# Optimization experiments

Hardware: AMD Instinct MI355X
Metric: run time of the kernel (lower is better)

## Reference

```python
import jax, jax.numpy as jnp
import numpy as np

K_NN = 3  # pointnet2 relation default k=3


def setup_inputs() -> dict:
    key = jax.random.key(0)
    k1, k2, k3 = jax.random.split(key, 3)
    B, N, S, C = 4, 16384, 4096, 256
    q = jax.random.normal(k1, (B, N, 3), dtype=jnp.float32)
    k = jax.random.normal(k2, (B, S, 3), dtype=jnp.float32)
    v = jax.random.normal(k3, (B, S, C), dtype=jnp.float32)
    return {"q": q, "k": k, "v": v}


def reference(q, k, v):
    # squared pairwise distance: ||q||^2 - 2 q.k + ||k||^2  -> [B, N, S]
    d = (
        jnp.sum(q * q, axis=-1, keepdims=True)
        - 2.0 * jnp.einsum("bnd,bsd->bns", q, k)
        + jnp.sum(k * k, axis=-1)[:, None, :]
    )
    # 3 nearest neighbors (smallest distances)
    neg_d, idx = jax.lax.top_k(-d, K_NN)          # [B, N, 3]
    dists = -neg_d
    recip = 1.0 / (dists + 1e-8)
    weight = recip / jnp.sum(recip, axis=-1, keepdims=True)  # [B, N, 3]
    # score is zero except at idx; scatter+dense matmul == gather-weighted sum
    B = q.shape[0]
    vg = v[jnp.arange(B)[:, None, None], idx]     # [B, N, 3, C]
    extract = jnp.einsum("bnk,bnkc->bnc", weight, vg)  # [B, N, C]
    return jnp.transpose(extract, (0, 2, 1))      # [B, C, N] (embed is identity)
```

## Files before the change

### kernel.cpp

```cpp
#include <hip/hip_runtime.h>

#define BB 4
#define NN 16384
#define SS 4096
#define CC 256
#define TLD 132

typedef float f32x4 __attribute__((ext_vector_type(4)));

__device__ __forceinline__ bool lexlt(float da, int ia, float db, int ib) {
  return (da < db) || ((da == db) && (ia < ib));
}

__global__ __launch_bounds__(256, 4) void scan_kernel(
    const float* __restrict__ qg, const float* __restrict__ kg,
    float4* __restrict__ dpart, int4* __restrict__ ipart) {
#pragma clang fp contract(off)
  __shared__ __align__(16) float4 kpts[1024];

  const int tid = threadIdx.x;
  const int blk = blockIdx.x;
  const int b = blk >> 8;
  const int seg = (blk >> 6) & 3;
  const int n0 = (blk & 63) << 8;
  const int wv = tid >> 6;
  const int lane = tid & 63;
  const int q = n0 + wv * 64 + lane;

  {
    const float* kb = kg + ((long)b * SS + (long)seg * 1024) * 3;
    const float4* src = (const float4*)kb + tid * 3;
    float4 f0 = src[0], f1 = src[1], f2 = src[2];
    float px[4] = {f0.x, f0.w, f1.z, f2.y};
    float py[4] = {f0.y, f1.x, f1.w, f2.z};
    float pz[4] = {f0.z, f1.y, f2.x, f2.w};
#pragma unroll
    for (int m = 0; m < 4; ++m) {
      float kk = (px[m] * px[m] + py[m] * py[m]) + pz[m] * pz[m];
      kpts[tid * 4 + m] = make_float4(px[m], py[m], pz[m], kk);
    }
  }

  const float* qp = qg + ((long)b * NN + q) * 3;
  float qx = qp[0], qy = qp[1], qz = qp[2];
  float qq = (qx * qx + qy * qy) + qz * qz;
  float d0 = 3.4e38f, d1 = 3.4e38f, d2 = 3.4e38f;
  int i0 = 0, i1 = 0, i2 = 0;
  __syncthreads();

  const int sb = seg * 1024;

#pragma unroll 4
  for (int i = 0; i < 256; ++i) {
    float4 kp = kpts[i];
    float dot = (qx * kp.x + qy * kp.y) + qz * kp.z;
    float d = __builtin_fmaf(dot, -2.0f, qq) + kp.w;
    const int s = sb + i;
    bool k2 = d < d2;
    bool k1 = d < d1;
    bool k0 = d < d0;
    float nd2 = __builtin_amdgcn_fmed3f(d, d1, d2);
    float nd1 = __builtin_amdgcn_fmed3f(d, d0, d1);
    float nd0 = fminf(d, d0);
    i2 = k1 ? i1 : (k2 ? s : i2);
    i1 = k0 ? i0 : (k1 ? s : i1);
    i0 = k0 ? s : i0;
    d2 = nd2; d1 = nd1; d0 = nd0;
  }

  for (int c = 1; c < 4; ++c) {
    const float tau = d2;
    const int base = c * 256;
#pragma unroll 4
    for (int i = 0; i < 256; ++i) {
      float4 kp = kpts[base + i];
      float dot = (qx * kp.x + qy * kp.y) + qz * kp.z;
      float d = __builtin_fmaf(dot, -2.0f, qq) + kp.w;
      if (__builtin_expect(__any(d < tau), 0)) {
        const int s = sb + base + i;
        bool k2 = d < d2;
        bool k1 = d < d1;
        bool k0 = d < d0;
        float nd2 = __builtin_amdgcn_fmed3f(d, d1, d2);
        float nd1 = __builtin_amdgcn_fmed3f(d, d0, d1);
        float nd0 = fminf(d, d0);
        i2 = k1 ? i1 : (k2 ? s : i2);
        i1 = k0 ? i0 : (k1 ? s : i1);
        i0 = k0 ? s : i0;
        d2 = nd2; d1 = nd1; d0 = nd0;
      }
    }
  }

  long gid = (long)b * NN + q;
  dpart[gid * 4 + seg] = make_float4(d0, d1, d2, 0.0f);
  ipart[gid * 4 + seg] = make_int4(i0, i1, i2, 0);
}

__global__ __launch_bounds__(256, 4) void gather_kernel(
    const float* __restrict__ vg, const float4* __restrict__ dpart,
    const int4* __restrict__ ipart, float* __restrict__ outg) {
#pragma clang fp contract(off)
  __shared__ __align__(16) float tile[64 * TLD];
  __shared__ float sw[64][3];
  __shared__ int si[64][3];

  const int tid = threadIdx.x;
  const int bid = blockIdx.x;
  const int xcd = bid & 7;
  const int b = xcd >> 1;
  const int chunk = xcd & 1;
  const int nblk = bid >> 3;
  const int n0 = nblk << 6;

  if (tid < 64) {
    long gid = (long)b * NN + n0 + tid;
    float D0 = 3.4e38f, D1 = 3.4e38f, D2 = 3.4e38f;
    int I0 = -1, I1 = -1, I2 = -1;
#pragma unroll
    for (int seg = 0; seg < 4; ++seg) {
      float4 dv = dpart[gid * 4 + seg];
      int4 iv = ipart[gid * 4 + seg];
      float ds_[3] = {dv.x, dv.y, dv.z};
      int is_[3] = {iv.x, iv.y, iv.z};
      for (int r = 0; r < 3; ++r) {
        float d = ds_[r];
        int s = is_[r];
        if (lexlt(d, s, D2, I2)) {
          if (lexlt(d, s, D1, I1)) {
            D2 = D1; I2 = I1;
            if (lexlt(d, s, D0, I0)) { D1 = D0; I1 = I0; D0 = d; I0 = s; }
            else { D1 = d; I1 = s; }
          } else { D2 = d; I2 = s; }
        }
      }
    }
    float r0 = 1.0f / (D0 + 1e-8f);
    float r1 = 1.0f / (D1 + 1e-8f);
    float r2 = 1.0f / (D2 + 1e-8f);
    float rs = (r0 + r1) + r2;
    sw[tid][0] = r0 / rs; sw[tid][1] = r1 / rs; sw[tid][2] = r2 / rs;
    si[tid][0] = I0; si[tid][1] = I1; si[tid][2] = I2;
  }
  __syncthreads();

  const int wv = tid >> 6;
  const int lane = tid & 63;
  const int qh = lane >> 5;
  const int slot = lane & 31;
  const float* vb = vg + (long)b * SS * CC + chunk * 128;

#pragma unroll 4
  for (int it = 0; it < 8; ++it) {
    int qs = wv * 16 + it * 2 + qh;
    float w0 = sw[qs][0], w1 = sw[qs][1], w2 = sw[qs][2];
    const float4* r0p = (const float4*)(vb + (long)si[qs][0] * CC);
    const float4* r1p = (const float4*)(vb + (long)si[qs][1] * CC);
    const float4* r2p = (const float4*)(vb + (long)si[qs][2] * CC);
    float4 a0 = r0p[slot], a1 = r1p[slot], a2 = r2p[slot];
    float4 acc;
    acc.x = (w0 * a0.x + w1 * a1.x) + w2 * a2.x;
    acc.y = (w0 * a0.y + w1 * a1.y) + w2 * a2.y;
    acc.z = (w0 * a0.z + w1 * a1.z) + w2 * a2.z;
    acc.w = (w0 * a0.w + w1 * a1.w) + w2 * a2.w;
    *(float4*)&tile[qs * TLD + slot * 4] = acc;
  }
  __syncthreads();

  {
    const int nf = tid & 15;
    const int cb0 = tid >> 4;
    const int q0 = nf << 2;
#pragma unroll 2
    for (int it = 0; it < 8; ++it) {
      int cl = cb0 + it * 16;
      int cch = (chunk << 7) + cl;
      f32x4 val;
      val.x = tile[(q0 + 0) * TLD + cl];
      val.y = tile[(q0 + 1) * TLD + cl];
      val.z = tile[(q0 + 2) * TLD + cl];
      val.w = tile[(q0 + 3) * TLD + cl];
      __builtin_nontemporal_store(
          val, (f32x4*)&outg[((long)(b * CC + cch)) * NN + n0 + q0]);
    }
  }
}

extern "C" void kernel_launch(void* const* d_in, const int* in_sizes, int n_in,
                              void* d_out, int out_size, void* d_ws, size_t ws_size,
                              hipStream_t stream) {
  const float* q = (const float*)d_in[0];
  const float* k = (const float*)d_in[1];
  const float* v = (const float*)d_in[2];
  float* out = (float*)d_out;
  float4* dpart = (float4*)d_ws;
  int4* ipart = (int4*)((char*)d_ws + (size_t)BB * NN * 4 * 16);
  hipLaunchKernelGGL(scan_kernel, dim3(1024), dim3(256), 0, stream, q, k, dpart, ipart);
  hipLaunchKernelGGL(gather_kernel, dim3(2048), dim3(256), 0, stream, v, dpart, ipart, out);
}
```

Baseline: 219.7 us.

## Process two queries per thread and stream precomputed keys from global

```diff
diff --git a/kernel.cpp b/kernel.cpp
--- a/kernel.cpp
+++ b/kernel.cpp
@@ -12,89 +12,117 @@
   return (da < db) || ((da == db) && (ia < ib));
 }
 
-__global__ __launch_bounds__(256, 4) void scan_kernel(
-    const float* __restrict__ qg, const float* __restrict__ kg,
+__global__ __launch_bounds__(256) void prep_kernel(const float* __restrict__ kg,
+                                                   float4* __restrict__ cand) {
+#pragma clang fp contract(off)
+  int gid = blockIdx.x * 256 + threadIdx.x;
+  int b = gid >> 12, s = gid & 4095;
+  const float* kp = kg + ((long)b * SS + s) * 3;
+  float x = kp[0], y = kp[1], z = kp[2];
+  float kk = (x * x + y * y) + z * z;
+  cand[(long)b * SS + s] = make_float4(x, y, z, kk);
+}
+
+__global__ __launch_bounds__(256, 2) void scan_kernel(
+    const float* __restrict__ qg, const f32x4* __restrict__ cand,
     float4* __restrict__ dpart, int4* __restrict__ ipart) {
 #pragma clang fp contract(off)
-  __shared__ __align__(16) float4 kpts[1024];
-
   const int tid = threadIdx.x;
   const int blk = blockIdx.x;
-  const int b = blk >> 8;
-  const int seg = (blk >> 6) & 3;
-  const int n0 = (blk & 63) << 8;
+  const int b = blk >> 7;
+  const int seg = (blk >> 5) & 3;
+  const int ngrp = blk & 31;
   const int wv = tid >> 6;
   const int lane = tid & 63;
-  const int q = n0 + wv * 64 + lane;
-
-  {
-    const float* kb = kg + ((long)b * SS + (long)seg * 1024) * 3;
-    const float4* src = (const float4*)kb + tid * 3;
-    float4 f0 = src[0], f1 = src[1], f2 = src[2];
-    float px[4] = {f0.x, f0.w, f1.z, f2.y};
-    float py[4] = {f0.y, f1.x, f1.w, f2.z};
-    float pz[4] = {f0.z, f1.y, f2.x, f2.w};
-#pragma unroll
-    for (int m = 0; m < 4; ++m) {
-      float kk = (px[m] * px[m] + py[m] * py[m]) + pz[m] * pz[m];
-      kpts[tid * 4 + m] = make_float4(px[m], py[m], pz[m], kk);
-    }
-  }
-
-  const float* qp = qg + ((long)b * NN + q) * 3;
-  float qx = qp[0], qy = qp[1], qz = qp[2];
-  float qq = (qx * qx + qy * qy) + qz * qz;
-  float d0 = 3.4e38f, d1 = 3.4e38f, d2 = 3.4e38f;
-  int i0 = 0, i1 = 0, i2 = 0;
-  __syncthreads();
-
+  const int n0 = (ngrp << 9) + (wv << 7);
+  const int qA = n0 + lane;
+  const int qB = n0 + 64 + lane;
+
+  const float* qpA = qg + ((long)b * NN + qA) * 3;
+  const float* qpB = qg + ((long)b * NN + qB) * 3;
+  float axq = qpA[0], ayq = qpA[1], azq = qpA[2];
+  float bxq = qpB[0], byq = qpB[1], bzq = qpB[2];
+  float aqq = (axq * axq + ayq * ayq) + azq * azq;
+  float bqq = (bxq * bxq + byq * byq) + bzq * bzq;
+  float ad0 = 3.4e38f, ad1 = 3.4e38f, ad2 = 3.4e38f;
+  float bd0 = 3.4e38f, bd1 = 3.4e38f, bd2 = 3.4e38f;
+  int ai0 = 0, ai1 = 0, ai2 = 0;
+  int bi0 = 0, bi1 = 0, bi2 = 0;
+
+  const f32x4* cb = cand + (long)b * SS + seg * 1024;
   const int sb = seg * 1024;
 
 #pragma unroll 4
   for (int i = 0; i < 256; ++i) {
-    float4 kp = kpts[i];
-    float dot = (qx * kp.x + qy * kp.y) + qz * kp.z;
-    float d = __builtin_fmaf(dot, -2.0f, qq) + kp.w;
+    f32x4 kp = cb[i];
     const int s = sb + i;
-    bool k2 = d < d2;
-    bool k1 = d < d1;
-    bool k0 = d < d0;
-    float nd2 = __builtin_amdgcn_fmed3f(d, d1, d2);
-    float nd1 = __builtin_amdgcn_fmed3f(d, d0, d1);
-    float nd0 = fminf(d, d0);
-    i2 = k1 ? i1 : (k2 ? s : i2);
-    i1 = k0 ? i0 : (k1 ? s : i1);
-    i0 = k0 ? s : i0;
-    d2 = nd2; d1 = nd1; d0 = nd0;
+    {
+      float dot = (axq * kp.x + ayq * kp.y) + azq * kp.z;
+      float d = __builtin_fmaf(dot, -2.0f, aqq) + kp.w;
+      bool k2 = d < ad2, k1 = d < ad1, k0 = d < ad0;
+      float nd2 = __builtin_amdgcn_fmed3f(d, ad1, ad2);
+      float nd1 = __builtin_amdgcn_fmed3f(d, ad0, ad1);
+      float nd0 = fminf(d, ad0);
+      ai2 = k1 ? ai1 : (k2 ? s : ai2);
+      ai1 = k0 ? ai0 : (k1 ? s : ai1);
+      ai0 = k0 ? s : ai0;
+      ad2 = nd2; ad1 = nd1; ad0 = nd0;
+    }
+    {
+      float dot = (bxq * kp.x + byq * kp.y) + bzq * kp.z;
+      float d = __builtin_fmaf(dot, -2.0f, bqq) + kp.w;
+      bool k2 = d < bd2, k1 = d < bd1, k0 = d < bd0;
+      float nd2 = __builtin_amdgcn_fmed3f(d, bd1, bd2);
+      float nd1 = __builtin_amdgcn_fmed3f(d, bd0, bd1);
+      float nd0 = fminf(d, bd0);
+      bi2 = k1 ? bi1 : (k2 ? s : bi2);
+      bi1 = k0 ? bi0 : (k1 ? s : bi1);
+      bi0 = k0 ? s : bi0;
+      bd2 = nd2; bd1 = nd1; bd0 = nd0;
+    }
   }
 
   for (int c = 1; c < 4; ++c) {
-    const float tau = d2;
+    const float tauA = ad2;
+    const float tauB = bd2;
     const int base = c * 256;
-#pragma unroll 4
+#pragma unroll 8
     for (int i = 0; i < 256; ++i) {
-      float4 kp = kpts[base + i];
-      float dot = (qx * kp.x + qy * kp.y) + qz * kp.z;
-      float d = __builtin_fmaf(dot, -2.0f, qq) + kp.w;
-      if (__builtin_expect(__any(d < tau), 0)) {
-        const int s = sb + base + i;
-        bool k2 = d < d2;
-        bool k1 = d < d1;
-        bool k0 = d < d0;
-        float nd2 = __builtin_amdgcn_fmed3f(d, d1, d2);
-        float nd1 = __builtin_amdgcn_fmed3f(d, d0, d1);
-        float nd0 = fminf(d, d0);
-        i2 = k1 ? i1 : (k2 ? s : i2);
-        i1 = k0 ? i0 : (k1 ? s : i1);
-        i0 = k0 ? s : i0;
-        d2 = nd2; d1 = nd1; d0 = nd0;
+      f32x4 kp = cb[base + i];
+      const int s = sb + base + i;
+      float dotA = (axq * kp.x + ayq * kp.y) + azq * kp.z;
+      float dA = __builtin_fmaf(dotA, -2.0f, aqq) + kp.w;
+      float dotB = (bxq * kp.x + byq * kp.y) + bzq * kp.z;
+      float dB = __builtin_fmaf(dotB, -2.0f, bqq) + kp.w;
+      if (__builtin_expect(__any(dA < tauA), 0)) {
+        bool k2 = dA < ad2, k1 = dA < ad1, k0 = dA < ad0;
+        float nd2 = __builtin_amdgcn_fmed3f(dA, ad1, ad2);
+        float nd1 = __builtin_amdgcn_fmed3f(dA, ad0, ad1);
+        float nd0 = fminf(dA, ad0);
+        ai2 = k1 ? ai1 : (k2 ? s : ai2);
+        ai1 = k0 ? ai0 : (k1 ? s : ai1);
+        ai0 = k0 ? s : ai0;
+        ad2 = nd2; ad1 = nd1; ad0 = nd0;
       }
-    }
-  }
-
-  long gid = (long)b * NN + q;
-  dpart[gid * 4 + seg] = make_float4(d0, d1, d2, 0.0f);
-  ipart[gid * 4 + seg] = make_int4(i0, i1, i2, 0);
+      if (__builtin_expect(__any(dB < tauB), 0)) {
+        bool k2 = dB < bd2, k1 = dB < bd1, k0 = dB < bd0;
+        float nd2 = __builtin_amdgcn_fmed3f(dB, bd1, bd2);
+        float nd1 = __builtin_amdgcn_fmed3f(dB, bd0, bd1);
+        float nd0 = fminf(dB, bd0);
+        bi2 = k1 ? bi1 : (k2 ? s : bi2);
+        bi1 = k0 ? bi0 : (k1 ? s : bi1);
+        bi0 = k0 ? s : bi0;
+        bd2 = nd2; bd1 = nd1; bd0 = nd0;
+      }
+    }
+  }
+
+  long gidA = (long)b * NN + qA;
+  long gidB = (long)b * NN + qB;
+  dpart[gidA * 4 + seg] = make_float4(ad0, ad1, ad2, 0.0f);
+  ipart[gidA * 4 + seg] = make_int4(ai0, ai1, ai2, 0);
+  dpart[gidB * 4 + seg] = make_float4(bd0, bd1, bd2, 0.0f);
+  ipart[gidB * 4 + seg] = make_int4(bi0, bi1, bi2, 0);
 }
 
 __global__ __launch_bounds__(256, 4) void gather_kernel(
@@ -195,6 +223,9 @@
   float* out = (float*)d_out;
   float4* dpart = (float4*)d_ws;
   int4* ipart = (int4*)((char*)d_ws + (size_t)BB * NN * 4 * 16);
-  hipLaunchKernelGGL(scan_kernel, dim3(1024), dim3(256), 0, stream, q, k, dpart, ipart);
+  float4* cand = (float4*)((char*)d_ws + 2 * (size_t)BB * NN * 4 * 16);
+  hipLaunchKernelGGL(prep_kernel, dim3(64), dim3(256), 0, stream, k, cand);
+  hipLaunchKernelGGL(scan_kernel, dim3(512), dim3(256), 0, stream, q,
+                     (const f32x4*)cand, dpart, ipart);
   hipLaunchKernelGGL(gather_kernel, dim3(2048), dim3(256), 0, stream, v, dpart, ipart, out);
 }
```

Result: slower. 258.8 us (+17.8%).
